# Kernel tuning notes

Measured on AMD Instinct MI355X. Metric: run time of the kernel, lower is better.

The kernel has to match this reference:

```python
import jax, jax.numpy as jnp
import numpy as np

B, N, DIM = 2, 2048, 2048
H, DH = 16, 128            # heads, dim_head; dim_inner = H*DH = 2048
SOFTCAP = 50.0
SCALE = DH ** -0.5


def setup_inputs() -> dict:
    key = jax.random.key(0)
    k1, k2, k3, k4 = jax.random.split(key, 4)
    s = 1.0 / np.sqrt(DIM)
    x = jax.random.normal(k1, (B, N, DIM), dtype=jnp.float32)
    w_qkv = jax.random.normal(k2, (DIM, 3 * H * DH), dtype=jnp.float32) * s
    w_gates = jax.random.normal(k3, (DIM, H), dtype=jnp.float32) * s
    w_out = jax.random.normal(k4, (H * DH, DIM), dtype=jnp.float32) * s
    return {"x": x, "w_qkv": w_qkv, "w_gates": w_gates, "w_out": w_out}


def reference(x, w_qkv, w_gates, w_out):
    b, n, _ = x.shape
    # to_qkv: Linear then 'b n (qkv h d) -> qkv b h n d'
    qkv = (x @ w_qkv).reshape(b, n, 3, H, DH).transpose(2, 0, 3, 1, 4)
    q, k, v = qkv[0], qkv[1], qkv[2]            # each [b, h, n, d]
    q = q * SCALE
    sim = jnp.einsum('bhid,bhjd->bhij', q, k)   # [b, h, n, n]
    sim = jnp.tanh(sim / SOFTCAP) * SOFTCAP     # softclamp
    mask_value = -jnp.finfo(sim.dtype).max
    causal_mask = jnp.triu(jnp.ones((n, n), dtype=bool), 1)
    sim = jnp.where(causal_mask, mask_value, sim)
    attn = jax.nn.softmax(sim, axis=-1)         # dropout = 0.0 (eval)
    out = jnp.einsum('bhij,bhjd->bhid', attn, v)
    # gating: 'b n h -> b h n 1' then sigmoid
    gates = jax.nn.sigmoid(x @ w_gates)         # [b, n, h]
    out = out * gates.transpose(0, 2, 1)[..., None]
    # to_out: 'b h n d -> b n (h d)' then Linear
    out = out.transpose(0, 2, 1, 3).reshape(b, n, H * DH) @ w_out
    return out
```

## Files before the change

### kernel.cpp

```cpp
#include <hip/hip_runtime.h>
#include <hip/hip_bf16.h>
#include <math.h>


typedef __attribute__((ext_vector_type(8))) __bf16 bf16x8;
typedef __attribute__((ext_vector_type(4))) __bf16 bf16x4;
typedef __attribute__((ext_vector_type(4))) float f32x4;

#define MFMA_BF16(a, b, c) __builtin_amdgcn_mfma_f32_16x16x32_bf16((a), (b), (c), 0, 0, 0)

#define NB 2
#define NSEQ 2048
#define NDIM 2048
#define NH 16
#define NDH 128
#define SCALE_Q 0.08838834764831845f

#define AS1 __attribute__((address_space(1)))
#define AS3 __attribute__((address_space(3)))
static __device__ __forceinline__ void gload_lds16(const void* g, void* l) {
  __builtin_amdgcn_global_load_lds((AS1 const void*)g, (AS3 void*)l, 16, 0, 0);
}

static __device__ __forceinline__ unsigned pack2_bf16(float a, float b) {
  unsigned short ua = __builtin_bit_cast(unsigned short, (__bf16)a);
  unsigned short ub = __builtin_bit_cast(unsigned short, (__bf16)b);
  return (unsigned)ua | ((unsigned)ub << 16);
}

__global__ __launch_bounds__(256) void cvt_bf16_kernel(const float* __restrict__ in,
                                                       __bf16* __restrict__ out) {
  int i = blockIdx.x * 256 + threadIdx.x;
  float4 v = reinterpret_cast<const float4*>(in)[i];
  bf16x4 o;
  o[0] = (__bf16)v.x; o[1] = (__bf16)v.y; o[2] = (__bf16)v.z; o[3] = (__bf16)v.w;
  reinterpret_cast<bf16x4*>(out)[i] = o;
}

__global__ __launch_bounds__(256) void transpose_cvt_kernel(const float* __restrict__ in,
                                                            __bf16* __restrict__ out,
                                                            int K, int C) {
  __shared__ float tile[32][33];
  int c0 = blockIdx.x * 32, k0 = blockIdx.y * 32;
  int t = threadIdx.x;
  int lc = t & 31, lr = t >> 5;
#pragma unroll
  for (int rr = 0; rr < 4; ++rr)
    tile[lr + rr * 8][lc] = in[(size_t)(k0 + lr + rr * 8) * C + c0 + lc];
  __syncthreads();
#pragma unroll
  for (int rr = 0; rr < 4; ++rr)
    out[(size_t)(c0 + lr + rr * 8) * K + k0 + lc] = (__bf16)tile[lc][lr + rr * 8];
}

struct SmemQ {
  __bf16 T[3][640][32];
};

static __device__ __forceinline__ const bf16x8* fragq(const __bf16* base, int row, int g) {
  return (const bf16x8*)(base + row * 32 + (g ^ ((row >> 1) & 3)) * 8);
}

__global__ __launch_bounds__(512, 2) void gemm_qkv256b(const __bf16* __restrict__ A,
                                                       const __bf16* __restrict__ Bt,
                                                       __bf16* __restrict__ qb,
                                                       __bf16* __restrict__ kb,
                                                       __bf16* __restrict__ vtb) {
  __shared__ __align__(1024) SmemQ S;
  int sblk = blockIdx.x;
  int x = sblk & 7, i = sblk >> 3;
  int m0 = (i >> 1) * 256;
  int n0 = (2 * x + (i & 1)) * 384;
  const __bf16* Ab = A + (size_t)m0 * 2048;
  const __bf16* Bb = Bt + (size_t)n0 * 2048;

  int tid = threadIdx.x;
  int w = tid >> 6, lane = tid & 63;
  int ln15 = lane & 15, g = lane >> 4;
  int wr = w >> 2, wc = w & 3;
  int lr4 = lane >> 2, l3 = lane & 3;

  auto stage = [&](int kt, int rb) {
#pragma unroll
    for (int j = 0; j < 5; ++j) {
      int k = w + 8 * j;
      int row = k * 16 + lr4;
      int sg = l3 ^ ((row >> 1) & 3);
      const __bf16* src = (k < 16)
          ? Ab + (size_t)row * 2048 + kt * 32 + sg * 8
          : Bb + (size_t)(row - 256) * 2048 + kt * 32 + sg * 8;
      gload_lds16(src, &S.T[rb][k * 16][0]);
    }
  };

  f32x4 acc[8][6];
#pragma unroll
  for (int a = 0; a < 8; ++a)
#pragma unroll
    for (int nf = 0; nf < 6; ++nf) acc[a][nf] = (f32x4){0.f, 0.f, 0.f, 0.f};

  stage(0, 0);
  stage(1, 1);
  for (int t = 0; t < 64; ++t) {
    int rb = t % 3;
    asm volatile("s_waitcnt vmcnt(5)" ::: "memory");
    __builtin_amdgcn_s_barrier();
    asm volatile("" ::: "memory");
    int ts = (t < 62) ? t + 2 : 63;
    stage(ts, (t + 2) % 3);
    const __bf16* Sb = &S.T[rb][0][0];
    bf16x8 bfr[6];
#pragma unroll
    for (int nf = 0; nf < 6; ++nf) {
      int row = 256 + wc * 96 + nf * 16 + ln15;
      bfr[nf] = *fragq(Sb, row, g);
    }
#pragma unroll
    for (int mh = 0; mh < 2; ++mh) {
      bf16x8 af[4];
#pragma unroll
      for (int a = 0; a < 4; ++a) {
        int row = wr * 128 + (mh * 4 + a) * 16 + ln15;
        af[a] = *fragq(Sb, row, g);
      }
      __builtin_amdgcn_s_setprio(1);
#pragma unroll
      for (int a = 0; a < 4; ++a)
#pragma unroll
        for (int nf = 0; nf < 6; ++nf)
          acc[mh * 4 + a][nf] = MFMA_BF16(af[a], bfr[nf], acc[mh * 4 + a][nf]);
      __builtin_amdgcn_s_setprio(0);
    }
  }
  asm volatile("s_waitcnt vmcnt(0)" ::: "memory");

#pragma unroll
  for (int nf = 0; nf < 6; ++nf) {
    int ng = n0 + wc * 96 + nf * 16 + ln15;
    int qkv = ng >> 11;
    int h = (ng >> 7) & 15;
    int d = ng & 127;
#pragma unroll
    for (int mf = 0; mf < 8; ++mf)
#pragma unroll
      for (int rr = 0; rr < 4; ++rr) {
        int m = m0 + wr * 128 + mf * 16 + g * 4 + rr;
        int b = m >> 11, n = m & 2047;
        int bh = b * NH + h;
        float v = acc[mf][nf][rr];
        if (qkv == 0)
          qb[((size_t)bh * NSEQ + n) * NDH + d] = (__bf16)(v * SCALE_Q);
        else if (qkv == 1)
          kb[((size_t)bh * NSEQ + n) * NDH + d] = (__bf16)v;
        else
          vtb[((size_t)bh * NDH + d) * NSEQ + n] = (__bf16)v;
      }
  }
}

template <int BN> struct SmemG {
  __bf16 A[2][2][128][32];
  __bf16 B[2][2][BN][32];
};

template <int BN>
static __device__ __forceinline__ void stage_half(const __bf16* __restrict__ Ab,
                                                  const __bf16* __restrict__ Bb,
                                                  SmemG<BN>* S, int buf, int ks,
                                                  int kt, int w, int lane) {
  constexpr int LB = BN / 128;
  {
    int gid = w * 64 + lane;
    int row = gid >> 2, gc = gid & 3;
    int sg = gc ^ ((row >> 1) & 3);
    gload_lds16(Ab + (size_t)row * 2048 + kt * 64 + ks * 32 + sg * 8,
                &S->A[buf][ks][0][0] + (size_t)(w * 64) * 8);
  }
#pragma unroll
  for (int j = 0; j < LB; ++j) {
    int gid = j * 512 + w * 64 + lane;
    int row = gid >> 2, gc = gid & 3;
    int sg = gc ^ ((row >> 1) & 3);
    gload_lds16(Bb + (size_t)row * 2048 + kt * 64 + ks * 32 + sg * 8,
                &S->B[buf][ks][0][0] + (size_t)(j * 512 + w * 64) * 8);
  }
}

static __device__ __forceinline__ const bf16x8* fragp(const __bf16* base, int row, int g) {
  return (const bf16x8*)(base + row * 32 + (g ^ ((row >> 1) & 3)) * 8);
}

template <int BN>
static __device__ __forceinline__ void gemm128_core(const __bf16* __restrict__ Abase,
                                                    const __bf16* __restrict__ Bbase,
                                                    SmemG<BN>* S,
                                                    f32x4 (*acc)[BN / 64]) {
  constexpr int NF = BN / 64;
  constexpr int LB = BN / 128;
  int tid = threadIdx.x;
  int w = tid >> 6, lane = tid & 63;
  int ln15 = lane & 15, g = lane >> 4;
  int wr = w >> 2, wc = w & 3;

#pragma unroll
  for (int i = 0; i < 4; ++i)
#pragma unroll
    for (int j = 0; j < NF; ++j) acc[i][j] = (f32x4){0.f, 0.f, 0.f, 0.f};

  stage_half<BN>(Abase, Bbase, S, 0, 0, 0, w, lane);
  stage_half<BN>(Abase, Bbase, S, 0, 1, 0, w, lane);

  for (int t = 0; t < 32; ++t) {
    int bf = t & 1, tb = bf ^ 1;
    int ts = (t < 31) ? t + 1 : 31;
#pragma unroll
    for (int ks = 0; ks < 2; ++ks) {
      stage_half<BN>(Abase, Bbase, S, tb, ks, ts, w, lane);
      if constexpr (LB == 3)
        asm volatile("s_waitcnt vmcnt(8)" ::: "memory");
      else
        asm volatile("s_waitcnt vmcnt(6)" ::: "memory");
      __builtin_amdgcn_s_barrier();
      const __bf16* SA = &S->A[bf][ks][0][0];
      const __bf16* SB = &S->B[bf][ks][0][0];
      bf16x8 af[4], bfr[NF];
#pragma unroll
      for (int nf = 0; nf < NF; ++nf) {
        int row = wc * (BN / 4) + nf * 16 + ln15;
        bfr[nf] = *fragp(SB, row, g);
      }
#pragma unroll
      for (int mf = 0; mf < 4; ++mf) {
        int row = wr * 64 + mf * 16 + ln15;
        af[mf] = *fragp(SA, row, g);
      }
      __builtin_amdgcn_s_setprio(1);
#pragma unroll
      for (int mf = 0; mf < 4; ++mf)
#pragma unroll
        for (int nf = 0; nf < NF; ++nf)
          acc[mf][nf] = MFMA_BF16(af[mf], bfr[nf], acc[mf][nf]);
      __builtin_amdgcn_s_setprio(0);
    }
  }
  asm volatile("s_waitcnt vmcnt(0)" ::: "memory");
}

__global__ __launch_bounds__(512) void gemm_out128(const __bf16* __restrict__ A,
                                                   const __bf16* __restrict__ Bt,
                                                   float* __restrict__ out) {
  __shared__ __align__(1024) SmemG<256> S;
  int sblk = blockIdx.x;
  int x = sblk & 7, i = sblk >> 3;
  int m0 = i * 128;
  int n0 = x * 256;
  f32x4 acc[4][4];
  gemm128_core<256>(A + (size_t)m0 * 2048, Bt + (size_t)n0 * 2048, &S, acc);

  int tid = threadIdx.x;
  int w = tid >> 6, lane = tid & 63;
  int ln15 = lane & 15, g = lane >> 4;
  int wr = w >> 2, wc = w & 3;
#pragma unroll
  for (int mf = 0; mf < 4; ++mf)
#pragma unroll
    for (int nf = 0; nf < 4; ++nf)
#pragma unroll
      for (int rr = 0; rr < 4; ++rr) {
        int m = m0 + wr * 64 + mf * 16 + g * 4 + rr;
        int c = n0 + wc * 64 + nf * 16 + ln15;
        out[(size_t)m * NDIM + c] = acc[mf][nf][rr];
      }
}

__global__ __launch_bounds__(256) void gates_kernel(const float* __restrict__ x,
                                                    const float* __restrict__ wg,
                                                    float* __restrict__ gates) {
  __shared__ float red[64];
  int row = blockIdx.x;
  int tid = threadIdx.x;
  float acc[16];
#pragma unroll
  for (int h = 0; h < 16; ++h) acc[h] = 0.f;
  const float* xr = x + (size_t)row * NDIM;
  for (int k = tid; k < NDIM; k += 256) {
    float xv = xr[k];
    const float* wr = wg + (size_t)k * NH;
#pragma unroll
    for (int h = 0; h < 16; ++h) acc[h] += xv * wr[h];
  }
  int w = tid >> 6, lane = tid & 63;
#pragma unroll
  for (int h = 0; h < 16; ++h) {
    float v = acc[h];
#pragma unroll
    for (int off = 32; off; off >>= 1) v += __shfl_down(v, off);
    if (lane == 0) red[w * 16 + h] = v;
  }
  __syncthreads();
  if (tid < 16) {
    float s = red[tid] + red[16 + tid] + red[32 + tid] + red[48 + tid];
    int b = row >> 11, n = row & 2047;
    gates[((size_t)(b * NH + tid)) * NSEQ + n] = 1.f / (1.f + expf(-s));
  }
}

static __device__ __forceinline__ void softcap_p(const f32x4* accS, float (*p)[4],
                                                 float& l_r, int j0, int q0s,
                                                 bool diag, int ln15, int g) {
#pragma unroll
  for (int jt = 0; jt < 4; ++jt)
#pragma unroll
    for (int r = 0; r < 4; ++r) {
      float e2 = __expf(accS[jt][r] * 0.04f);
      float cap = 50.f - __fdividef(100.f, e2 + 1.f);
      float pv = __expf(cap - 12.f);
      if (diag && (j0 + jt * 16 + g * 4 + r > q0s + ln15)) pv = 0.f;
      p[jt][r] = pv;
      l_r += pv;
    }
}

static __device__ __forceinline__ bf16x8 build_pa(const float (*p)[4], int c,
                                                  int lane_lo, int lane_hi, int g) {
  unsigned P0w0 = pack2_bf16(p[2 * c][0], p[2 * c][1]);
  unsigned P0w1 = pack2_bf16(p[2 * c][2], p[2 * c][3]);
  unsigned P1w0 = pack2_bf16(p[2 * c + 1][0], p[2 * c + 1][1]);
  unsigned P1w1 = pack2_bf16(p[2 * c + 1][2], p[2 * c + 1][3]);
  unsigned a0 = (unsigned)__shfl((int)P0w0, lane_lo);
  unsigned a1 = (unsigned)__shfl((int)P0w1, lane_lo);
  unsigned b0 = (unsigned)__shfl((int)P1w0, lane_lo);
  unsigned b1 = (unsigned)__shfl((int)P1w1, lane_lo);
  unsigned c0 = (unsigned)__shfl((int)P0w0, lane_hi);
  unsigned c1 = (unsigned)__shfl((int)P0w1, lane_hi);
  unsigned e0 = (unsigned)__shfl((int)P1w0, lane_hi);
  unsigned e1 = (unsigned)__shfl((int)P1w1, lane_hi);
  union { unsigned u[4]; bf16x8 v; } pu;
  pu.u[0] = (g < 2) ? a0 : b0;
  pu.u[1] = (g < 2) ? a1 : b1;
  pu.u[2] = (g < 2) ? c0 : e0;
  pu.u[3] = (g < 2) ? c1 : e1;
  return pu.v;
}

static __device__ __forceinline__ void attn_tile2(const __bf16* __restrict__ Kl,
                                                  const __bf16* __restrict__ Vl,
                                                  const bf16x8* qfh, const bf16x8* qfl,
                                                  f32x4* acc_h, f32x4* acc_l,
                                                  float& l_h, float& l_l,
                                                  int j0, int q0h, int q0l,
                                                  bool diag_h, bool diag_l, bool do_lo,
                                                  int ln15, int g) {
  f32x4 sh[4], sl[4];
#pragma unroll
  for (int jt = 0; jt < 4; ++jt) {
    sh[jt] = (f32x4){0.f, 0.f, 0.f, 0.f};
    sl[jt] = (f32x4){0.f, 0.f, 0.f, 0.f};
  }
  __builtin_amdgcn_s_setprio(1);
#pragma unroll
  for (int jt = 0; jt < 4; ++jt)
#pragma unroll
    for (int kc = 0; kc < 4; ++kc) {
      int row = jt * 16 + ln15;
      int bc = (kc * 64 + g * 16) ^ ((row & 7) << 4);
      bf16x8 kf = *reinterpret_cast<const bf16x8*>(Kl + row * 128 + (bc >> 1));
      sh[jt] = MFMA_BF16(kf, qfh[kc], sh[jt]);
      if (do_lo) sl[jt] = MFMA_BF16(kf, qfl[kc], sl[jt]);
    }
  __builtin_amdgcn_s_setprio(0);
  float ph[4][4], pl[4][4];
  softcap_p(sh, ph, l_h, j0, q0h, diag_h, ln15, g);
  if (do_lo) softcap_p(sl, pl, l_l, j0, q0l, diag_l, ln15, g);
  int lane_lo = ln15 + 32 * (g & 1);
  int lane_hi = lane_lo + 16;
#pragma unroll
  for (int c = 0; c < 2; ++c) {
    bf16x8 pah = build_pa(ph, c, lane_lo, lane_hi, g);
    bf16x8 pal = build_pa(pl, c, lane_lo, lane_hi, g);
    __builtin_amdgcn_s_setprio(1);
#pragma unroll
    for (int d0 = 0; d0 < 8; ++d0) {
      int d = d0 * 16 + ln15;
      int bc = (c * 64 + g * 16) ^ ((d & 7) << 4);
      bf16x8 vf = *reinterpret_cast<const bf16x8*>(Vl + d * 64 + (bc >> 1));
      acc_h[d0] = MFMA_BF16(pah, vf, acc_h[d0]);
      if (do_lo) acc_l[d0] = MFMA_BF16(pal, vf, acc_l[d0]);
    }
    __builtin_amdgcn_s_setprio(0);
  }
}

__global__ __launch_bounds__(256, 2) void attn_kernel(const __bf16* __restrict__ qb,
                                                      const __bf16* __restrict__ kb,
                                                      const __bf16* __restrict__ vtb,
                                                      const float* __restrict__ gates,
                                                      __bf16* __restrict__ og) {
  __shared__ __align__(1024) __bf16 Kl[2][64 * 128];
  __shared__ __align__(1024) __bf16 Vl[2][128 * 64];
  int tid = threadIdx.x;
  int w = tid >> 6, lane = tid & 63;
  int ln15 = lane & 15, g = lane >> 4;
  int bx = blockIdx.x;
  int lo = bx & 15, bh = bx >> 4;
  int hi = 31 - lo;
  const __bf16* qh = qb + (size_t)bh * NSEQ * NDH;
  const __bf16* kh = kb + (size_t)bh * NSEQ * NDH;
  const __bf16* vh = vtb + (size_t)bh * NDH * NSEQ;

  int q0h = hi * 64 + w * 16;
  int q0l = lo * 64 + w * 16;
  bf16x8 qfh[4], qfl[4];
#pragma unroll
  for (int kc = 0; kc < 4; ++kc) {
    qfh[kc] = *reinterpret_cast<const bf16x8*>(qh + (size_t)(q0h + ln15) * NDH + kc * 32 + g * 8);
    qfl[kc] = *reinterpret_cast<const bf16x8*>(qh + (size_t)(q0l + ln15) * NDH + kc * 32 + g * 8);
  }

  f32x4 acc_h[8], acc_l[8];
#pragma unroll
  for (int d0 = 0; d0 < 8; ++d0) {
    acc_h[d0] = (f32x4){0.f, 0.f, 0.f, 0.f};
    acc_l[d0] = (f32x4){0.f, 0.f, 0.f, 0.f};
  }
  float l_h = 0.f, l_l = 0.f;

  auto stage = [&](int t, int buf) {
    int j0 = t * 64;
#pragma unroll
    for (int i = 0; i < 4; ++i) {
      int gi = (i * 4 + w) * 64 + lane;
      int kr = gi >> 4, kcs = gi & 15;
      int kc_ = kcs ^ (kr & 7);
      gload_lds16(kh + (size_t)(j0 + kr) * NDH + kc_ * 8, &Kl[buf][(i * 4 + w) * 512]);
      int vr = gi >> 3, vcs = gi & 7;
      int vc_ = vcs ^ (vr & 7);
      gload_lds16(vh + (size_t)vr * NSEQ + j0 + vc_ * 8, &Vl[buf][(i * 4 + w) * 512]);
    }
  };

  stage(0, 0);
  for (int t = 0; t <= hi; ++t) {
    int cb = t & 1;
    if (t < hi) {
      stage(t + 1, cb ^ 1);
      asm volatile("s_waitcnt vmcnt(8)" ::: "memory");
    } else {
      asm volatile("s_waitcnt vmcnt(0)" ::: "memory");
    }
    __builtin_amdgcn_s_barrier();
    attn_tile2(&Kl[cb][0], &Vl[cb][0], qfh, qfl, acc_h, acc_l, l_h, l_l,
               t * 64, q0h, q0l, t == hi, t == lo, t <= lo, ln15, g);
    __builtin_amdgcn_s_barrier();
  }

  l_h += __shfl_xor(l_h, 16); l_h += __shfl_xor(l_h, 32);
  l_l += __shfl_xor(l_l, 16); l_l += __shfl_xor(l_l, 32);

  int b = bh >> 4, h = bh & 15;
#pragma unroll
  for (int set = 0; set < 2; ++set) {
    int q0s = set ? q0l : q0h;
    f32x4* acc = set ? acc_l : acc_h;
    float lr = set ? l_l : l_h;
    float gv[4];
#pragma unroll
    for (int r = 0; r < 4; ++r) {
      float lv = __shfl(lr, g * 4 + r);
      int row = q0s + g * 4 + r;
      gv[r] = gates[(size_t)bh * NSEQ + row] / lv;
    }
#pragma unroll
    for (int d0 = 0; d0 < 8; ++d0)
#pragma unroll
      for (int r = 0; r < 4; ++r) {
        int row = q0s + g * 4 + r;
        og[((size_t)(b * NSEQ + row)) * NDIM + h * NDH + d0 * 16 + ln15] =
            (__bf16)(acc[d0][r] * gv[r]);
      }
  }
}

extern "C" void kernel_launch(void* const* d_in, const int* in_sizes, int n_in,
                              void* d_out, int out_size, void* d_ws, size_t ws_size,
                              hipStream_t stream) {
  const float* x = (const float*)d_in[0];
  const float* w_qkv = (const float*)d_in[1];
  const float* w_gates = (const float*)d_in[2];
  const float* w_out = (const float*)d_in[3];
  float* out = (float*)d_out;
  char* ws = (char*)d_ws;

  __bf16* x_bf   = (__bf16*)(ws + 0);
  __bf16* wqkv_t = (__bf16*)(ws + 16777216);
  __bf16* wout_t = (__bf16*)(ws + 41943040);
  __bf16* q_buf  = (__bf16*)(ws + 50331648);
  __bf16* k_buf  = (__bf16*)(ws + 67108864);
  __bf16* vt_buf = (__bf16*)(ws + 83886080);
  float*  gates  = (float*)(ws + 100663296);
  __bf16* attn_g = (__bf16*)(ws + 100925440);

  cvt_bf16_kernel<<<8192, 256, 0, stream>>>(x, x_bf);
  transpose_cvt_kernel<<<dim3(192, 64), 256, 0, stream>>>(w_qkv, wqkv_t, 2048, 6144);
  transpose_cvt_kernel<<<dim3(64, 64), 256, 0, stream>>>(w_out, wout_t, 2048, 2048);
  gemm_qkv256b<<<256, 512, 0, stream>>>(x_bf, wqkv_t, q_buf, k_buf, vt_buf);
  gates_kernel<<<4096, 256, 0, stream>>>(x, w_gates, gates);
  attn_kernel<<<512, 256, 0, stream>>>(q_buf, k_buf, vt_buf, gates, attn_g);
  gemm_out128<<<256, 512, 0, stream>>>(attn_g, wout_t, out);
}
```

Baseline: 339.8 us.

## Split paired causal q-tiles into one tile per block with single-buffered LDS

The attention kernel previously processed two q-tiles per block (a high and a low tile, paired so the causal workload per block was balanced) with double-buffered K/V staging. It now assigns one q-tile per block, doubling the grid to 1024 blocks, drops the double buffer, and raises launch bounds to 4 waves per SIMD to increase occupancy. The K/V reuse across two q-tiles and the load/compute overlap are lost, so each tile load is fully exposed unless occupancy hides it. Blocks now carry unequal causal work, ordered heaviest first.

```diff
diff --git a/kernel.cpp b/kernel.cpp
--- a/kernel.cpp
+++ b/kernel.cpp
@@ -343,20 +343,14 @@
   return pu.v;
 }
 
-static __device__ __forceinline__ void attn_tile2(const __bf16* __restrict__ Kl,
+static __device__ __forceinline__ void attn_tile1(const __bf16* __restrict__ Kl,
                                                   const __bf16* __restrict__ Vl,
-                                                  const bf16x8* qfh, const bf16x8* qfl,
-                                                  f32x4* acc_h, f32x4* acc_l,
-                                                  float& l_h, float& l_l,
-                                                  int j0, int q0h, int q0l,
-                                                  bool diag_h, bool diag_l, bool do_lo,
-                                                  int ln15, int g) {
-  f32x4 sh[4], sl[4];
-#pragma unroll
-  for (int jt = 0; jt < 4; ++jt) {
-    sh[jt] = (f32x4){0.f, 0.f, 0.f, 0.f};
-    sl[jt] = (f32x4){0.f, 0.f, 0.f, 0.f};
-  }
+                                                  const bf16x8* qf, f32x4* acc,
+                                                  float& l_r, int j0, int q0,
+                                                  bool diag, int ln15, int g) {
+  f32x4 sh[4];
+#pragma unroll
+  for (int jt = 0; jt < 4; ++jt) sh[jt] = (f32x4){0.f, 0.f, 0.f, 0.f};
   __builtin_amdgcn_s_setprio(1);
 #pragma unroll
   for (int jt = 0; jt < 4; ++jt)
@@ -365,120 +359,97 @@
       int row = jt * 16 + ln15;
       int bc = (kc * 64 + g * 16) ^ ((row & 7) << 4);
       bf16x8 kf = *reinterpret_cast<const bf16x8*>(Kl + row * 128 + (bc >> 1));
-      sh[jt] = MFMA_BF16(kf, qfh[kc], sh[jt]);
-      if (do_lo) sl[jt] = MFMA_BF16(kf, qfl[kc], sl[jt]);
+      sh[jt] = MFMA_BF16(kf, qf[kc], sh[jt]);
     }
   __builtin_amdgcn_s_setprio(0);
-  float ph[4][4], pl[4][4];
-  softcap_p(sh, ph, l_h, j0, q0h, diag_h, ln15, g);
-  if (do_lo) softcap_p(sl, pl, l_l, j0, q0l, diag_l, ln15, g);
+  float p[4][4];
+  softcap_p(sh, p, l_r, j0, q0, diag, ln15, g);
   int lane_lo = ln15 + 32 * (g & 1);
   int lane_hi = lane_lo + 16;
 #pragma unroll
   for (int c = 0; c < 2; ++c) {
-    bf16x8 pah = build_pa(ph, c, lane_lo, lane_hi, g);
-    bf16x8 pal = build_pa(pl, c, lane_lo, lane_hi, g);
+    bf16x8 pa = build_pa(p, c, lane_lo, lane_hi, g);
     __builtin_amdgcn_s_setprio(1);
 #pragma unroll
     for (int d0 = 0; d0 < 8; ++d0) {
       int d = d0 * 16 + ln15;
       int bc = (c * 64 + g * 16) ^ ((d & 7) << 4);
       bf16x8 vf = *reinterpret_cast<const bf16x8*>(Vl + d * 64 + (bc >> 1));
-      acc_h[d0] = MFMA_BF16(pah, vf, acc_h[d0]);
-      if (do_lo) acc_l[d0] = MFMA_BF16(pal, vf, acc_l[d0]);
+      acc[d0] = MFMA_BF16(pa, vf, acc[d0]);
     }
     __builtin_amdgcn_s_setprio(0);
   }
 }
 
-__global__ __launch_bounds__(256, 2) void attn_kernel(const __bf16* __restrict__ qb,
+__global__ __launch_bounds__(256, 4) void attn_kernel(const __bf16* __restrict__ qb,
                                                       const __bf16* __restrict__ kb,
                                                       const __bf16* __restrict__ vtb,
                                                       const float* __restrict__ gates,
                                                       __bf16* __restrict__ og) {
-  __shared__ __align__(1024) __bf16 Kl[2][64 * 128];
-  __shared__ __align__(1024) __bf16 Vl[2][128 * 64];
+  __shared__ __align__(1024) __bf16 Kl[64 * 128];
+  __shared__ __align__(1024) __bf16 Vl[128 * 64];
   int tid = threadIdx.x;
   int w = tid >> 6, lane = tid & 63;
   int ln15 = lane & 15, g = lane >> 4;
   int bx = blockIdx.x;
-  int lo = bx & 15, bh = bx >> 4;
-  int hi = 31 - lo;
+  int qt = 31 - (bx & 31);
+  int bh = bx >> 5;
   const __bf16* qh = qb + (size_t)bh * NSEQ * NDH;
   const __bf16* kh = kb + (size_t)bh * NSEQ * NDH;
   const __bf16* vh = vtb + (size_t)bh * NDH * NSEQ;
 
-  int q0h = hi * 64 + w * 16;
-  int q0l = lo * 64 + w * 16;
-  bf16x8 qfh[4], qfl[4];
-#pragma unroll
-  for (int kc = 0; kc < 4; ++kc) {
-    qfh[kc] = *reinterpret_cast<const bf16x8*>(qh + (size_t)(q0h + ln15) * NDH + kc * 32 + g * 8);
-    qfl[kc] = *reinterpret_cast<const bf16x8*>(qh + (size_t)(q0l + ln15) * NDH + kc * 32 + g * 8);
-  }
-
-  f32x4 acc_h[8], acc_l[8];
-#pragma unroll
-  for (int d0 = 0; d0 < 8; ++d0) {
-    acc_h[d0] = (f32x4){0.f, 0.f, 0.f, 0.f};
-    acc_l[d0] = (f32x4){0.f, 0.f, 0.f, 0.f};
-  }
-  float l_h = 0.f, l_l = 0.f;
-
-  auto stage = [&](int t, int buf) {
+  int q0 = qt * 64 + w * 16;
+  bf16x8 qf[4];
+#pragma unroll
+  for (int kc = 0; kc < 4; ++kc)
+    qf[kc] = *reinterpret_cast<const bf16x8*>(qh + (size_t)(q0 + ln15) * NDH + kc * 32 + g * 8);
+
+  f32x4 acc[8];
+#pragma unroll
+  for (int d0 = 0; d0 < 8; ++d0) acc[d0] = (f32x4){0.f, 0.f, 0.f, 0.f};
+  float l_r = 0.f;
+
+  auto stage = [&](int t) {
     int j0 = t * 64;
 #pragma unroll
     for (int i = 0; i < 4; ++i) {
       int gi = (i * 4 + w) * 64 + lane;
       int kr = gi >> 4, kcs = gi & 15;
       int kc_ = kcs ^ (kr & 7);
-      gload_lds16(kh + (size_t)(j0 + kr) * NDH + kc_ * 8, &Kl[buf][(i * 4 + w) * 512]);
+      gload_lds16(kh + (size_t)(j0 + kr) * NDH + kc_ * 8, &Kl[(i * 4 + w) * 512]);
       int vr = gi >> 3, vcs = gi & 7;
       int vc_ = vcs ^ (vr & 7);
-      gload_lds16(vh + (size_t)vr * NSEQ + j0 + vc_ * 8, &Vl[buf][(i * 4 + w) * 512]);
+      gload_lds16(vh + (size_t)vr * NSEQ + j0 + vc_ * 8, &Vl[(i * 4 + w) * 512]);
     }
   };
 
-  stage(0, 0);
-  for (int t = 0; t <= hi; ++t) {
-    int cb = t & 1;
-    if (t < hi) {
-      stage(t + 1, cb ^ 1);
-      asm volatile("s_waitcnt vmcnt(8)" ::: "memory");
-    } else {
-      asm volatile("s_waitcnt vmcnt(0)" ::: "memory");
-    }
+  for (int t = 0; t <= qt; ++t) {
     __builtin_amdgcn_s_barrier();
-    attn_tile2(&Kl[cb][0], &Vl[cb][0], qfh, qfl, acc_h, acc_l, l_h, l_l,
-               t * 64, q0h, q0l, t == hi, t == lo, t <= lo, ln15, g);
+    stage(t);
+    asm volatile("s_waitcnt vmcnt(0)" ::: "memory");
     __builtin_amdgcn_s_barrier();
-  }
-
-  l_h += __shfl_xor(l_h, 16); l_h += __shfl_xor(l_h, 32);
-  l_l += __shfl_xor(l_l, 16); l_l += __shfl_xor(l_l, 32);
+    attn_tile1(Kl, Vl, qf, acc, l_r, t * 64, q0, t == qt, ln15, g);
+  }
+
+  l_r += __shfl_xor(l_r, 16);
+  l_r += __shfl_xor(l_r, 32);
 
   int b = bh >> 4, h = bh & 15;
-#pragma unroll
-  for (int set = 0; set < 2; ++set) {
-    int q0s = set ? q0l : q0h;
-    f32x4* acc = set ? acc_l : acc_h;
-    float lr = set ? l_l : l_h;
-    float gv[4];
+  float gv[4];
+#pragma unroll
+  for (int r = 0; r < 4; ++r) {
+    float lv = __shfl(l_r, g * 4 + r);
+    int row = q0 + g * 4 + r;
+    gv[r] = gates[(size_t)bh * NSEQ + row] / lv;
+  }
+#pragma unroll
+  for (int d0 = 0; d0 < 8; ++d0)
 #pragma unroll
     for (int r = 0; r < 4; ++r) {
-      float lv = __shfl(lr, g * 4 + r);
-      int row = q0s + g * 4 + r;
-      gv[r] = gates[(size_t)bh * NSEQ + row] / lv;
-    }
-#pragma unroll
-    for (int d0 = 0; d0 < 8; ++d0)
-#pragma unroll
-      for (int r = 0; r < 4; ++r) {
-        int row = q0s + g * 4 + r;
-        og[((size_t)(b * NSEQ + row)) * NDIM + h * NDH + d0 * 16 + ln15] =
-            (__bf16)(acc[d0][r] * gv[r]);
-      }
-  }
+      int row = q0 + g * 4 + r;
+      og[((size_t)(b * NSEQ + row)) * NDIM + h * NDH + d0 * 16 + ln15] =
+          (__bf16)(acc[d0][r] * gv[r]);
+    }
 }
 
 extern "C" void kernel_launch(void* const* d_in, const int* in_sizes, int n_in,
@@ -505,6 +476,6 @@
   transpose_cvt_kernel<<<dim3(64, 64), 256, 0, stream>>>(w_out, wout_t, 2048, 2048);
   gemm_qkv256b<<<256, 512, 0, stream>>>(x_bf, wqkv_t, q_buf, k_buf, vt_buf);
   gates_kernel<<<4096, 256, 0, stream>>>(x, w_gates, gates);
-  attn_kernel<<<512, 256, 0, stream>>>(q_buf, k_buf, vt_buf, gates, attn_g);
+  attn_kernel<<<1024, 256, 0, stream>>>(q_buf, k_buf, vt_buf, gates, attn_g);
   gemm_out128<<<256, 512, 0, stream>>>(attn_g, wout_t, out);
 }
```

Result: slower. 369.9 us (+8.9%).

## Fuse x conversion with gate projection; use 512-thread attention blocks over 128-row tiles

Applied to the files above, without the earlier changes.

The x-to-bf16 conversion and the gate projection now run in one kernel, so x is read once and a launch is dropped. The attention kernel moves to 512-thread blocks, each covering a 128-row high and a 128-row low query tile per head. Each wave decides per key tile whether its rows need work (do_hi/do_lo) and computes its own diagonal masking. The larger block halves the grid and reuses each staged K/V tile across 8 waves, at the cost of more causal imbalance between waves inside a block.

```diff
diff --git a/kernel.cpp b/kernel.cpp
--- a/kernel.cpp
+++ b/kernel.cpp
@@ -28,13 +28,46 @@
   return (unsigned)ua | ((unsigned)ub << 16);
 }
 
-__global__ __launch_bounds__(256) void cvt_bf16_kernel(const float* __restrict__ in,
-                                                       __bf16* __restrict__ out) {
-  int i = blockIdx.x * 256 + threadIdx.x;
-  float4 v = reinterpret_cast<const float4*>(in)[i];
-  bf16x4 o;
-  o[0] = (__bf16)v.x; o[1] = (__bf16)v.y; o[2] = (__bf16)v.z; o[3] = (__bf16)v.w;
-  reinterpret_cast<bf16x4*>(out)[i] = o;
+__global__ __launch_bounds__(256) void cvt_gates_kernel(const float* __restrict__ x,
+                                                        const float* __restrict__ wg,
+                                                        __bf16* __restrict__ x_bf,
+                                                        float* __restrict__ gates) {
+  __shared__ float red[64];
+  int row = blockIdx.x;
+  int tid = threadIdx.x;
+  const float* xr = x + (size_t)row * NDIM;
+  int k0 = tid * 8;
+  float4 v0 = *reinterpret_cast<const float4*>(xr + k0);
+  float4 v1 = *reinterpret_cast<const float4*>(xr + k0 + 4);
+  float vv[8] = {v0.x, v0.y, v0.z, v0.w, v1.x, v1.y, v1.z, v1.w};
+  union { bf16x8 v; } o;
+#pragma unroll
+  for (int j = 0; j < 8; ++j) o.v[j] = (__bf16)vv[j];
+  *reinterpret_cast<bf16x8*>(x_bf + (size_t)row * NDIM + k0) = o.v;
+
+  float acc[16];
+#pragma unroll
+  for (int h = 0; h < 16; ++h) acc[h] = 0.f;
+#pragma unroll
+  for (int j = 0; j < 8; ++j) {
+    const float* wr = wg + (size_t)(k0 + j) * NH;
+#pragma unroll
+    for (int h = 0; h < 16; ++h) acc[h] += vv[j] * wr[h];
+  }
+  int w = tid >> 6, lane = tid & 63;
+#pragma unroll
+  for (int h = 0; h < 16; ++h) {
+    float v = acc[h];
+#pragma unroll
+    for (int off = 32; off; off >>= 1) v += __shfl_down(v, off);
+    if (lane == 0) red[w * 16 + h] = v;
+  }
+  __syncthreads();
+  if (tid < 16) {
+    float s = red[tid] + red[16 + tid] + red[32 + tid] + red[48 + tid];
+    int b = row >> 11, n = row & 2047;
+    gates[((size_t)(b * NH + tid)) * NSEQ + n] = 1.f / (1.f + expf(-s));
+  }
 }
 
 __global__ __launch_bounds__(256) void transpose_cvt_kernel(const float* __restrict__ in,
@@ -271,38 +304,6 @@
         int c = n0 + wc * 64 + nf * 16 + ln15;
         out[(size_t)m * NDIM + c] = acc[mf][nf][rr];
       }
-}
-
-__global__ __launch_bounds__(256) void gates_kernel(const float* __restrict__ x,
-                                                    const float* __restrict__ wg,
-                                                    float* __restrict__ gates) {
-  __shared__ float red[64];
-  int row = blockIdx.x;
-  int tid = threadIdx.x;
-  float acc[16];
-#pragma unroll
-  for (int h = 0; h < 16; ++h) acc[h] = 0.f;
-  const float* xr = x + (size_t)row * NDIM;
-  for (int k = tid; k < NDIM; k += 256) {
-    float xv = xr[k];
-    const float* wr = wg + (size_t)k * NH;
-#pragma unroll
-    for (int h = 0; h < 16; ++h) acc[h] += xv * wr[h];
-  }
-  int w = tid >> 6, lane = tid & 63;
-#pragma unroll
-  for (int h = 0; h < 16; ++h) {
-    float v = acc[h];
-#pragma unroll
-    for (int off = 32; off; off >>= 1) v += __shfl_down(v, off);
-    if (lane == 0) red[w * 16 + h] = v;
-  }
-  __syncthreads();
-  if (tid < 16) {
-    float s = red[tid] + red[16 + tid] + red[32 + tid] + red[48 + tid];
-    int b = row >> 11, n = row & 2047;
-    gates[((size_t)(b * NH + tid)) * NSEQ + n] = 1.f / (1.f + expf(-s));
-  }
 }
 
 static __device__ __forceinline__ void softcap_p(const f32x4* accS, float (*p)[4],
@@ -349,7 +350,8 @@
                                                   f32x4* acc_h, f32x4* acc_l,
                                                   float& l_h, float& l_l,
                                                   int j0, int q0h, int q0l,
-                                                  bool diag_h, bool diag_l, bool do_lo,
+                                                  bool diag_h, bool diag_l,
+                                                  bool do_hi, bool do_lo,
                                                   int ln15, int g) {
   f32x4 sh[4], sl[4];
 #pragma unroll
@@ -365,12 +367,12 @@
       int row = jt * 16 + ln15;
       int bc = (kc * 64 + g * 16) ^ ((row & 7) << 4);
       bf16x8 kf = *reinterpret_cast<const bf16x8*>(Kl + row * 128 + (bc >> 1));
-      sh[jt] = MFMA_BF16(kf, qfh[kc], sh[jt]);
+      if (do_hi) sh[jt] = MFMA_BF16(kf, qfh[kc], sh[jt]);
       if (do_lo) sl[jt] = MFMA_BF16(kf, qfl[kc], sl[jt]);
     }
   __builtin_amdgcn_s_setprio(0);
   float ph[4][4], pl[4][4];
-  softcap_p(sh, ph, l_h, j0, q0h, diag_h, ln15, g);
+  if (do_hi) softcap_p(sh, ph, l_h, j0, q0h, diag_h, ln15, g);
   if (do_lo) softcap_p(sl, pl, l_l, j0, q0l, diag_l, ln15, g);
   int lane_lo = ln15 + 32 * (g & 1);
   int lane_hi = lane_lo + 16;
@@ -384,14 +386,14 @@
       int d = d0 * 16 + ln15;
       int bc = (c * 64 + g * 16) ^ ((d & 7) << 4);
       bf16x8 vf = *reinterpret_cast<const bf16x8*>(Vl + d * 64 + (bc >> 1));
-      acc_h[d0] = MFMA_BF16(pah, vf, acc_h[d0]);
+      if (do_hi) acc_h[d0] = MFMA_BF16(pah, vf, acc_h[d0]);
       if (do_lo) acc_l[d0] = MFMA_BF16(pal, vf, acc_l[d0]);
     }
     __builtin_amdgcn_s_setprio(0);
   }
 }
 
-__global__ __launch_bounds__(256, 2) void attn_kernel(const __bf16* __restrict__ qb,
+__global__ __launch_bounds__(512, 2) void attn_kernel(const __bf16* __restrict__ qb,
                                                       const __bf16* __restrict__ kb,
                                                       const __bf16* __restrict__ vtb,
                                                       const float* __restrict__ gates,
@@ -402,14 +404,14 @@
   int w = tid >> 6, lane = tid & 63;
   int ln15 = lane & 15, g = lane >> 4;
   int bx = blockIdx.x;
-  int lo = bx & 15, bh = bx >> 4;
-  int hi = 31 - lo;
+  int p = bx & 7, bh = bx >> 3;
+  int hi = 15 - p, lo = p;
   const __bf16* qh = qb + (size_t)bh * NSEQ * NDH;
   const __bf16* kh = kb + (size_t)bh * NSEQ * NDH;
   const __bf16* vh = vtb + (size_t)bh * NDH * NSEQ;
 
-  int q0h = hi * 64 + w * 16;
-  int q0l = lo * 64 + w * 16;
+  int q0h = hi * 128 + w * 16;
+  int q0l = lo * 128 + w * 16;
   bf16x8 qfh[4], qfl[4];
 #pragma unroll
   for (int kc = 0; kc < 4; ++kc) {
@@ -428,29 +430,36 @@
   auto stage = [&](int t, int buf) {
     int j0 = t * 64;
 #pragma unroll
-    for (int i = 0; i < 4; ++i) {
-      int gi = (i * 4 + w) * 64 + lane;
+    for (int c = 0; c < 2; ++c) {
+      int gi = c * 512 + w * 64 + lane;
       int kr = gi >> 4, kcs = gi & 15;
       int kc_ = kcs ^ (kr & 7);
-      gload_lds16(kh + (size_t)(j0 + kr) * NDH + kc_ * 8, &Kl[buf][(i * 4 + w) * 512]);
+      gload_lds16(kh + (size_t)(j0 + kr) * NDH + kc_ * 8,
+                  &Kl[buf][(c * 512 + w * 64) * 8]);
       int vr = gi >> 3, vcs = gi & 7;
       int vc_ = vcs ^ (vr & 7);
-      gload_lds16(vh + (size_t)vr * NSEQ + j0 + vc_ * 8, &Vl[buf][(i * 4 + w) * 512]);
+      gload_lds16(vh + (size_t)vr * NSEQ + j0 + vc_ * 8,
+                  &Vl[buf][(c * 512 + w * 64) * 8]);
     }
   };
 
+  int ntiles = 2 * hi + 2;
   stage(0, 0);
-  for (int t = 0; t <= hi; ++t) {
+  for (int t = 0; t < ntiles; ++t) {
     int cb = t & 1;
-    if (t < hi) {
+    if (t < ntiles - 1) {
       stage(t + 1, cb ^ 1);
-      asm volatile("s_waitcnt vmcnt(8)" ::: "memory");
+      asm volatile("s_waitcnt vmcnt(4)" ::: "memory");
     } else {
       asm volatile("s_waitcnt vmcnt(0)" ::: "memory");
     }
     __builtin_amdgcn_s_barrier();
+    int j0 = t * 64;
+    bool do_hi = (j0 <= q0h + 15);
+    bool do_lo = (j0 <= q0l + 15);
     attn_tile2(&Kl[cb][0], &Vl[cb][0], qfh, qfl, acc_h, acc_l, l_h, l_l,
-               t * 64, q0h, q0l, t == hi, t == lo, t <= lo, ln15, g);
+               j0, q0h, q0l, j0 + 63 > q0h, j0 + 63 > q0l, do_hi, do_lo,
+               ln15, g);
     __builtin_amdgcn_s_barrier();
   }
 
@@ -500,11 +509,10 @@
   float*  gates  = (float*)(ws + 100663296);
   __bf16* attn_g = (__bf16*)(ws + 100925440);
 
-  cvt_bf16_kernel<<<8192, 256, 0, stream>>>(x, x_bf);
+  cvt_gates_kernel<<<4096, 256, 0, stream>>>(x, w_gates, x_bf, gates);
   transpose_cvt_kernel<<<dim3(192, 64), 256, 0, stream>>>(w_qkv, wqkv_t, 2048, 6144);
   transpose_cvt_kernel<<<dim3(64, 64), 256, 0, stream>>>(w_out, wout_t, 2048, 2048);
   gemm_qkv256b<<<256, 512, 0, stream>>>(x_bf, wqkv_t, q_buf, k_buf, vt_buf);
-  gates_kernel<<<4096, 256, 0, stream>>>(x, w_gates, gates);
-  attn_kernel<<<512, 256, 0, stream>>>(q_buf, k_buf, vt_buf, gates, attn_g);
+  attn_kernel<<<256, 512, 0, stream>>>(q_buf, k_buf, vt_buf, gates, attn_g);
   gemm_out128<<<256, 512, 0, stream>>>(attn_g, wout_t, out);
 }
```

Result: slower. 381.4 us (+12.2%).
